# Performance work log

Measured on AMD Instinct MI355X. Metric: run time of the kernel, lower is better.

## Reference

```python
import jax, jax.numpy as jnp
import numpy as np

HIDDEN = 2048
N_HEADS = 16
N_KV_HEADS = 4
HEAD_DIM = HIDDEN // N_HEADS  # 128
ROPE_THETA = 10000.0
BATCH = 2
SEQ = 2048


def setup_inputs() -> dict:
    key = jax.random.key(0)
    k1, k2, k3, k4, k5 = jax.random.split(key, 5)
    s = 0.02
    return {
        "hidden_states": jax.random.normal(k1, (BATCH, SEQ, HIDDEN), dtype=jnp.float32),
        "attention_mask": jnp.zeros((BATCH, 1, 1, SEQ), dtype=jnp.float32),
        "Wq": jax.random.normal(k2, (HIDDEN, N_HEADS * HEAD_DIM), dtype=jnp.float32) * s,
        "Wk": jax.random.normal(k3, (HIDDEN, N_KV_HEADS * HEAD_DIM), dtype=jnp.float32) * s,
        "Wv": jax.random.normal(k4, (HIDDEN, N_KV_HEADS * HEAD_DIM), dtype=jnp.float32) * s,
        "Wo": jax.random.normal(k5, (N_HEADS * HEAD_DIM, HIDDEN), dtype=jnp.float32) * s,
    }


def _rope_cos_sin(seq_len, dtype):
    inv_freq = 1.0 / (ROPE_THETA ** (jnp.arange(0, HEAD_DIM, 2, dtype=jnp.float32) / HEAD_DIM))
    t = jnp.arange(seq_len, dtype=jnp.float32)
    freqs = t[:, None] * inv_freq[None, :]            # [S, D/2]
    emb = jnp.concatenate([freqs, freqs], axis=-1)    # [S, D]
    cos = jnp.cos(emb)[None, None, :, :].astype(dtype)  # [1,1,S,D]
    sin = jnp.sin(emb)[None, None, :, :].astype(dtype)
    return cos, sin


def _apply_rope(x, cos, sin):
    # x: [B,H,S,D]; faithful to torch code: rotated = cat((-x[...,1::2], x[...,::2]), -1)
    x1 = x[..., ::2]
    x2 = x[..., 1::2]
    rotated = jnp.concatenate([-x2, x1], axis=-1)
    return x * cos + rotated * sin


def reference(hidden_states, attention_mask, Wq, Wk, Wv, Wo):
    B, S, _ = hidden_states.shape
    scale = HEAD_DIM ** -0.5

    q = (hidden_states @ Wq).reshape(B, S, N_HEADS, HEAD_DIM).transpose(0, 2, 1, 3)      # [B,H,S,D]
    k = (hidden_states @ Wk).reshape(B, S, N_KV_HEADS, HEAD_DIM).transpose(0, 2, 1, 3)   # [B,KV,S,D]
    v = (hidden_states @ Wv).reshape(B, S, N_KV_HEADS, HEAD_DIM).transpose(0, 2, 1, 3)

    cos, sin = _rope_cos_sin(S, hidden_states.dtype)
    q = _apply_rope(q, cos, sin)
    k = _apply_rope(k, cos, sin)

    rep = N_HEADS // N_KV_HEADS
    k = jnp.repeat(k, rep, axis=1)  # [B,H,S,D]
    v = jnp.repeat(v, rep, axis=1)

    scores = jnp.einsum("bhqd,bhkd->bhqk", q, k) * scale  # [B,H,S,S]
    causal = jnp.tril(jnp.ones((S, S), dtype=bool))[None, None]
    scores = jnp.where(causal, scores, -jnp.inf)
    scores = scores + attention_mask  # additive float mask, broadcast [B,1,1,S]

    attn = jax.nn.softmax(scores, axis=-1)
    out = jnp.einsum("bhqk,bhkd->bhqd", attn, v)           # [B,H,S,D]
    out = out.transpose(0, 2, 1, 3).reshape(B, S, N_HEADS * HEAD_DIM)
    return out @ Wo
```

## Files before the change

### kernel.cpp

```cpp
#include <hip/hip_runtime.h>
#include <hip/hip_bf16.h>

#define BATCH 2
#define SEQ   2048
#define NH    16
#define NKV   4
#define HD    128
#define KDIM  2048
#define MROWS 4096
#define NQKV  3072

typedef __attribute__((ext_vector_type(8))) short  s16x8;
typedef __attribute__((ext_vector_type(4))) short  s16x4;
typedef __attribute__((ext_vector_type(4))) float  f32x4;
typedef __attribute__((ext_vector_type(8))) __bf16 b16x8;

#define BARRIER_LDS() do { \
    asm volatile("s_waitcnt lgkmcnt(0)" ::: "memory"); \
    __builtin_amdgcn_s_barrier(); \
  } while (0)

__device__ __forceinline__ unsigned short f2bf(float f) {
  __hip_bfloat16 h = __float2bfloat16(f);
  return *reinterpret_cast<unsigned short*>(&h);
}
__device__ __forceinline__ float bf2f(unsigned short h) {
  union { unsigned int u; float f; } x; x.u = ((unsigned int)h) << 16;
  return x.f;
}

__device__ __forceinline__ f32x4 MFMA16(s16x8 a, s16x8 b, f32x4 c) {
  return __builtin_amdgcn_mfma_f32_16x16x32_bf16(
      __builtin_bit_cast(b16x8, a), __builtin_bit_cast(b16x8, b), c, 0, 0, 0);
}

__device__ __forceinline__ void gload_lds16(const void* g, void* lds) {
  __builtin_amdgcn_global_load_lds(
      (const __attribute__((address_space(1))) void*)g,
      (__attribute__((address_space(3))) void*)lds, 16, 0, 0);
}

__global__ __launch_bounds__(256) void transpose_convert(
    const float* __restrict__ W, unsigned short* __restrict__ WT, int Kd, int Nd) {
  __shared__ float tile[32][33];
  int n0 = blockIdx.x * 32, k0 = blockIdx.y * 32;
  int tx = threadIdx.x & 31, ty = threadIdx.x >> 5;
#pragma unroll
  for (int i = 0; i < 4; ++i)
    tile[ty + i * 8][tx] = W[(size_t)(k0 + ty + i * 8) * Nd + n0 + tx];
  __syncthreads();
#pragma unroll
  for (int i = 0; i < 4; ++i)
    WT[(size_t)(n0 + ty + i * 8) * Kd + k0 + tx] = f2bf(tile[tx][ty + i * 8]);
}

__global__ __launch_bounds__(256) void conv_bf16(
    const float* __restrict__ X, unsigned short* __restrict__ Y) {
  int i = blockIdx.x * 256 + threadIdx.x;
  const float4 a = ((const float4*)X)[2 * i];
  const float4 b = ((const float4*)X)[2 * i + 1];
  s16x8 o;
  o[0] = (short)f2bf(a.x); o[1] = (short)f2bf(a.y);
  o[2] = (short)f2bf(a.z); o[3] = (short)f2bf(a.w);
  o[4] = (short)f2bf(b.x); o[5] = (short)f2bf(b.y);
  o[6] = (short)f2bf(b.z); o[7] = (short)f2bf(b.w);
  ((s16x8*)Y)[i] = o;
}

__global__ __launch_bounds__(256) void rope_table_kernel(float* __restrict__ tbl) {
  int i = blockIdx.x * 256 + threadIdx.x;
  int s = i >> 6, j = i & 63;
  float inv = powf(10000.0f, -(float)(2 * j) * (1.0f / 128.0f));
  float f = (float)s * inv;
  tbl[2 * i]     = cosf(f);
  tbl[2 * i + 1] = sinf(f);
}

__global__ __launch_bounds__(256) void gemm_qkv(
    const unsigned short* __restrict__ A, const unsigned short* __restrict__ BT,
    unsigned short* __restrict__ Qo, unsigned short* __restrict__ Ko,
    unsigned short* __restrict__ Vo) {
  __shared__ __align__(16) unsigned short la[128][32];
  __shared__ __align__(16) unsigned short lb[128][32];
  int tid = threadIdx.x, lane = tid & 63, w = tid >> 6;
  int lin = blockIdx.x;
  int swz = (lin & 7) * 96 + (lin >> 3);
  int bx = swz % 24, by = swz / 24;
  int m0 = by * 128, n0 = bx * 128;
  int wr = (w >> 1) * 64, wc = (w & 1) * 64;
  int fr = lane & 15, kg = (lane >> 4) * 8, rg = (lane >> 4) * 4;
  f32x4 acc[4][4] = {};
  for (int kt = 0; kt < KDIM; kt += 32) {
    __syncthreads();
#pragma unroll
    for (int i = 0; i < 2; ++i) {
      int idx = tid + i * 256;
      int row = idx >> 2, seg = idx & 3;
      gload_lds16(A + (size_t)(m0 + row) * KDIM + kt + seg * 8,
                  (char*)la + (size_t)(i * 256 + w * 64) * 16);
      gload_lds16(BT + (size_t)(n0 + row) * KDIM + kt + seg * 8,
                  (char*)lb + (size_t)(i * 256 + w * 64) * 16);
    }
    __syncthreads();
    s16x8 af[4], bf[4];
#pragma unroll
    for (int mi = 0; mi < 4; ++mi) af[mi] = *(const s16x8*)(&la[wr + mi * 16 + fr][kg]);
#pragma unroll
    for (int ni = 0; ni < 4; ++ni) bf[ni] = *(const s16x8*)(&lb[wc + ni * 16 + fr][kg]);
#pragma unroll
    for (int mi = 0; mi < 4; ++mi)
#pragma unroll
      for (int ni = 0; ni < 4; ++ni) acc[mi][ni] = MFMA16(af[mi], bf[ni], acc[mi][ni]);
  }
  int rbase = m0 + wr + rg;
#pragma unroll
  for (int ni = 0; ni < 4; ++ni) {
    int gn = n0 + wc + ni * 16 + fr;
    if (gn < 2048) {
      int hh = gn >> 7, d = gn & 127;
#pragma unroll
      for (int mi = 0; mi < 4; ++mi)
#pragma unroll
        for (int r = 0; r < 4; ++r) {
          int grow = rbase + mi * 16 + r;
          int bb = grow >> 11, ss = grow & 2047;
          Qo[((size_t)(bb * NH + hh) * SEQ + ss) * HD + d] = f2bf(acc[mi][ni][r]);
        }
    } else if (gn < 2560) {
      int c = gn - 2048, kvh = c >> 7, d = c & 127;
#pragma unroll
      for (int mi = 0; mi < 4; ++mi)
#pragma unroll
        for (int r = 0; r < 4; ++r) {
          int grow = rbase + mi * 16 + r;
          int bb = grow >> 11, ss = grow & 2047;
          Ko[((size_t)(bb * NKV + kvh) * SEQ + ss) * HD + d] = f2bf(acc[mi][ni][r]);
        }
    } else {
      int c = gn - 2560, kvh = c >> 7, d = c & 127;
#pragma unroll
      for (int mi = 0; mi < 4; ++mi) {
        int grow0 = rbase + mi * 16;
        int bb = grow0 >> 11, ss = grow0 & 2047;
        s16x4 pk;
#pragma unroll
        for (int r = 0; r < 4; ++r) pk[r] = (short)f2bf(acc[mi][ni][r]);
        *(s16x4*)(Vo + ((size_t)(bb * NKV + kvh) * HD + d) * SEQ + ss) = pk;
      }
    }
  }
}

__global__ __launch_bounds__(256) void gemm_out(
    const unsigned short* __restrict__ A, const unsigned short* __restrict__ BT,
    float* __restrict__ C) {
  __shared__ __align__(16) unsigned short la[128][32];
  __shared__ __align__(16) unsigned short lb[128][32];
  int tid = threadIdx.x, lane = tid & 63, w = tid >> 6;
  int lin = blockIdx.x;
  int swz = (lin & 7) * 64 + (lin >> 3);
  int bx = swz % 16, by = swz / 16;
  int m0 = by * 128, n0 = bx * 128;
  int wr = (w >> 1) * 64, wc = (w & 1) * 64;
  int fr = lane & 15, kg = (lane >> 4) * 8, rg = (lane >> 4) * 4;
  f32x4 acc[4][4] = {};
  for (int kt = 0; kt < KDIM; kt += 32) {
    __syncthreads();
#pragma unroll
    for (int i = 0; i < 2; ++i) {
      int idx = tid + i * 256;
      int row = idx >> 2, seg = idx & 3;
      gload_lds16(A + (size_t)(m0 + row) * KDIM + kt + seg * 8,
                  (char*)la + (size_t)(i * 256 + w * 64) * 16);
      gload_lds16(BT + (size_t)(n0 + row) * KDIM + kt + seg * 8,
                  (char*)lb + (size_t)(i * 256 + w * 64) * 16);
    }
    __syncthreads();
    s16x8 af[4], bf[4];
#pragma unroll
    for (int mi = 0; mi < 4; ++mi) af[mi] = *(const s16x8*)(&la[wr + mi * 16 + fr][kg]);
#pragma unroll
    for (int ni = 0; ni < 4; ++ni) bf[ni] = *(const s16x8*)(&lb[wc + ni * 16 + fr][kg]);
#pragma unroll
    for (int mi = 0; mi < 4; ++mi)
#pragma unroll
      for (int ni = 0; ni < 4; ++ni) acc[mi][ni] = MFMA16(af[mi], bf[ni], acc[mi][ni]);
  }
  int rbase = m0 + wr + rg;
#pragma unroll
  for (int ni = 0; ni < 4; ++ni) {
    int gn = n0 + wc + ni * 16 + fr;
#pragma unroll
    for (int mi = 0; mi < 4; ++mi)
#pragma unroll
      for (int r = 0; r < 4; ++r)
        C[(size_t)(rbase + mi * 16 + r) * 2048 + gn] = acc[mi][ni][r];
  }
}

__global__ __launch_bounds__(256) void rope2(
    unsigned short* __restrict__ X, const float* __restrict__ tbl) {
  __shared__ __align__(16) unsigned short xs[32][136];
  int tid = threadIdx.x;
  size_t r0 = (size_t)blockIdx.x * 32;
#pragma unroll
  for (int i = 0; i < 2; ++i) {
    int idx = tid + i * 256;
    int pr = idx >> 4, seg = idx & 15;
    *(s16x8*)(&xs[pr][seg * 8]) = *(const s16x8*)(X + (r0 + pr) * 128 + seg * 8);
  }
  __syncthreads();
  int pr = tid >> 3, jb = (tid & 7) * 8;
  size_t row = r0 + pr;
  int s = (int)(row & (SEQ - 1));
  s16x8 o0, o1;
#pragma unroll
  for (int j0 = 0; j0 < 8; ++j0) {
    int j = jb + j0;
    float c  = tbl[(s * 64 + j) * 2];
    float sn = tbl[(s * 64 + j) * 2 + 1];
    float xj   = bf2f(xs[pr][j]);
    float xj64 = bf2f(xs[pr][j + 64]);
    float x2j  = bf2f(xs[pr][2 * j]);
    float x2j1 = bf2f(xs[pr][2 * j + 1]);
    o0[j0] = (short)f2bf(xj * c - x2j1 * sn);
    o1[j0] = (short)f2bf(xj64 * c + x2j * sn);
  }
  unsigned short* xp = X + row * 128;
  *(s16x8*)(xp + jb)      = o0;
  *(s16x8*)(xp + 64 + jb) = o1;
}

__global__ __launch_bounds__(256, 2) void attn_fwd(
    const unsigned short* __restrict__ Q, const unsigned short* __restrict__ K,
    const unsigned short* __restrict__ VT, const float* __restrict__ mask,
    unsigned short* __restrict__ O) {
  __shared__ __align__(16) unsigned short kt_[64][136];
  __shared__ __align__(16) unsigned short vt_[128][68];
  __shared__ __align__(16) unsigned short pt_[4][16][36];

  int tid = threadIdx.x, lane = tid & 63, w = tid >> 6;
  int l = blockIdx.x;
  int grp = l & 7, slot = l >> 3;
  int hloc = slot & 3, qt = 31 - (slot >> 2);
  int b = grp >> 2, kvh = grp & 3, h = kvh * 4 + hloc;
  int qbase = qt * 64;
  int qw = qbase + w * 16;
  int fr = lane & 15, g = lane >> 4, kg = g * 8, rg = g * 4;

  const unsigned short* Qb = Q + (size_t)(b * NH + h) * SEQ * HD;
  const unsigned short* Kb = K + (size_t)(b * NKV + kvh) * SEQ * HD;
  const unsigned short* Vb = VT + (size_t)(b * NKV + kvh) * HD * SEQ;
  const float* mb = mask + (size_t)b * SEQ;

  int krow = tid >> 4, kpos = (tid & 15) * 8;
  const float sc2 = 0.12751744584812722f;
  const float L2E = 1.44269504088896f;
  int bS = b * SEQ;
  int ntiles = qt + 1;

  s16x8 aq[4];
#pragma unroll
  for (int dc = 0; dc < 4; ++dc)
    aq[dc] = *(const s16x8*)(Qb + (size_t)(qw + fr) * HD + dc * 32 + kg);

  f32x4 oacc[8] = {};
  float m_r = -3e38f, l_r = 0.f;

  s16x8 kreg[4], vreg[4];
#pragma unroll
  for (int i = 0; i < 4; ++i)
    kreg[i] = *(const s16x8*)(Kb + (size_t)(krow + i * 16) * HD + kpos);
#pragma unroll
  for (int i = 0; i < 4; ++i) {
    int c = tid + 256 * i;
    vreg[i] = *(const s16x8*)(Vb + (size_t)(c >> 3) * SEQ + (c & 7) * 8);
  }
#pragma unroll
  for (int i = 0; i < 4; ++i)
    *(s16x8*)(&kt_[krow + i * 16][kpos]) = kreg[i];
  BARRIER_LDS();

  for (int t = 0; t < ntiles; ++t) {
    int kv0 = t * 64;
    bool notlast = (t + 1 < ntiles);
    bool diag = (kv0 + 63 > qw);

#pragma unroll
    for (int i = 0; i < 4; ++i) {
      int c = tid + 256 * i;
      *(s16x8*)(&vt_[c >> 3][(c & 7) * 8]) = vreg[i];
    }
    if (notlast) {
#pragma unroll
      for (int i = 0; i < 4; ++i)
        kreg[i] = *(const s16x8*)(Kb + (size_t)(kv0 + 64 + krow + i * 16) * HD + kpos);
    }

    f32x4 sf[4];
    __builtin_amdgcn_s_setprio(1);
#pragma unroll
    for (int mk = 0; mk < 4; ++mk) {
      s16x8 ak[4];
#pragma unroll
      for (int dc = 0; dc < 4; ++dc)
        ak[dc] = *(const s16x8*)(&kt_[mk * 16 + fr][dc * 32 + kg]);
      sf[mk] = f32x4{0.f, 0.f, 0.f, 0.f};
#pragma unroll
      for (int dc = 0; dc < 4; ++dc)
        sf[mk] = MFMA16(ak[dc], aq[dc], sf[mk]);
    }
    __builtin_amdgcn_s_setprio(0);

#pragma unroll
    for (int mk = 0; mk < 4; ++mk) {
      float4 mv = *(const float4*)(mb + kv0 + mk * 16 + rg);
      float mvr[4] = {mv.x * L2E, mv.y * L2E, mv.z * L2E, mv.w * L2E};
      if (diag) {
#pragma unroll
        for (int r = 0; r < 4; ++r) {
          int kv = kv0 + mk * 16 + rg + r;
          float v = sf[mk][r] * sc2 + mvr[r];
          sf[mk][r] = (kv <= qw + fr) ? v : -3e38f;
        }
      } else {
#pragma unroll
        for (int r = 0; r < 4; ++r)
          sf[mk][r] = sf[mk][r] * sc2 + mvr[r];
      }
    }

    float pm01a = fmaxf(sf[0][0], sf[0][1]), pm01b = fmaxf(sf[0][2], sf[0][3]);
    float pm11a = fmaxf(sf[1][0], sf[1][1]), pm11b = fmaxf(sf[1][2], sf[1][3]);
    float pm21a = fmaxf(sf[2][0], sf[2][1]), pm21b = fmaxf(sf[2][2], sf[2][3]);
    float pm31a = fmaxf(sf[3][0], sf[3][1]), pm31b = fmaxf(sf[3][2], sf[3][3]);
    float pm0 = fmaxf(pm01a, pm01b), pm1 = fmaxf(pm11a, pm11b);
    float pm2 = fmaxf(pm21a, pm21b), pm3 = fmaxf(pm31a, pm31b);
    float pm = fmaxf(fmaxf(pm0, pm1), fmaxf(pm2, pm3));
    pm = fmaxf(pm, __shfl_xor(pm, 16, 64));
    pm = fmaxf(pm, __shfl_xor(pm, 32, 64));
    if (!__all(pm - m_r <= 8.0f)) {
      float mo = m_r;
      float mn = fmaxf(mo, pm);
      float al = exp2f(mo - mn);
      m_r = mn;
      l_r *= al;
#pragma unroll
      for (int r = 0; r < 4; ++r) {
        float ar = __shfl(al, rg + r, 16);
#pragma unroll
        for (int od = 0; od < 8; ++od) oacc[od][r] *= ar;
      }
    }
    float rs = 0.f;
#pragma unroll
    for (int mk = 0; mk < 4; ++mk)
#pragma unroll
      for (int r = 0; r < 4; ++r) {
        float ppv = exp2f(sf[mk][r] - m_r);
        sf[mk][r] = ppv;
        rs += ppv;
      }
    rs += __shfl_xor(rs, 16, 64);
    rs += __shfl_xor(rs, 32, 64);
    l_r += rs;

    BARRIER_LDS();

    if (notlast) {
#pragma unroll
      for (int i = 0; i < 4; ++i)
        *(s16x8*)(&kt_[krow + i * 16][kpos]) = kreg[i];
#pragma unroll
      for (int i = 0; i < 4; ++i) {
        int c = tid + 256 * i;
        vreg[i] = *(const s16x8*)(Vb + (size_t)(c >> 3) * SEQ + kv0 + 64 + (c & 7) * 8);
      }
    }

#pragma unroll
    for (int kk = 0; kk < 2; ++kk) {
#pragma unroll
      for (int mh = 0; mh < 2; ++mh) {
        int mk = kk * 2 + mh;
        s16x4 pk;
#pragma unroll
        for (int r = 0; r < 4; ++r) pk[r] = (short)f2bf(sf[mk][r]);
        *(s16x4*)(&pt_[w][fr][mh * 16 + rg]) = pk;
      }
      s16x8 ap = *(const s16x8*)(&pt_[w][fr][kg]);
      __builtin_amdgcn_s_setprio(1);
#pragma unroll
      for (int od = 0; od < 8; ++od) {
        s16x8 bv = *(const s16x8*)(&vt_[od * 16 + fr][kk * 32 + kg]);
        oacc[od] = MFMA16(ap, bv, oacc[od]);
      }
      __builtin_amdgcn_s_setprio(0);
    }
    BARRIER_LDS();
  }

  float iv = 1.0f / l_r;
  float ivr[4];
#pragma unroll
  for (int r = 0; r < 4; ++r) ivr[r] = __shfl(iv, rg + r, 16);
#pragma unroll
  for (int r = 0; r < 4; ++r) {
    unsigned short* op = O + (size_t)(bS + qw + rg + r) * 2048 + h * 128 + fr;
#pragma unroll
    for (int od = 0; od < 8; ++od)
      op[od * 16] = f2bf(oacc[od][r] * ivr[r]);
  }
}

extern "C" void kernel_launch(void* const* d_in, const int* in_sizes, int n_in,
                              void* d_out, int out_size, void* d_ws, size_t ws_size,
                              hipStream_t stream) {
  const float* hidden = (const float*)d_in[0];
  const float* mask   = (const float*)d_in[1];
  const float* Wq     = (const float*)d_in[2];
  const float* Wk     = (const float*)d_in[3];
  const float* Wv     = (const float*)d_in[4];
  const float* Wo     = (const float*)d_in[5];
  float* out = (float*)d_out;

  char* ws = (char*)d_ws;
  unsigned short* BT  = (unsigned short*)(ws);
  unsigned short* WoT = (unsigned short*)(ws + 12582912);
  unsigned short* Qb  = (unsigned short*)(ws + 20971520);
  unsigned short* Kb  = (unsigned short*)(ws + 37748736);
  unsigned short* VT  = (unsigned short*)(ws + 41943040);
  unsigned short* AO  = (unsigned short*)(ws + 46137344);
  float*          tbl = (float*)(ws + 62914560);
  unsigned short* Ab  = AO;

  conv_bf16<<<MROWS * KDIM / (256 * 8), 256, 0, stream>>>(hidden, Ab);
  transpose_convert<<<dim3(64, 64), 256, 0, stream>>>(Wq, BT, KDIM, 2048);
  transpose_convert<<<dim3(16, 64), 256, 0, stream>>>(Wk, BT + (size_t)2048 * KDIM, KDIM, 512);
  transpose_convert<<<dim3(16, 64), 256, 0, stream>>>(Wv, BT + (size_t)2560 * KDIM, KDIM, 512);
  transpose_convert<<<dim3(64, 64), 256, 0, stream>>>(Wo, WoT, KDIM, 2048);
  rope_table_kernel<<<512, 256, 0, stream>>>(tbl);

  gemm_qkv<<<dim3(768), 256, 0, stream>>>(Ab, BT, Qb, Kb, VT);
  rope2<<<(BATCH * NH * SEQ) / 32, 256, 0, stream>>>(Qb, tbl);
  rope2<<<(BATCH * NKV * SEQ) / 32, 256, 0, stream>>>(Kb, tbl);
  attn_fwd<<<dim3(1024), 256, 0, stream>>>(Qb, Kb, VT, mask, AO);
  gemm_out<<<dim3(512), 256, 0, stream>>>(AO, WoT, out);
}
```

Baseline: 229.3 us.

## Double-buffer K/V tiles in attention and merge weight-prep and rope launches

The attention kernel now keeps two LDS buffers for K and V. The next tile is written into the spare buffer while the current one is consumed, which removes one of the two block barriers per iteration. The four weight transpose launches are merged into a single grid, and the two rope launches into another, to cut launch overhead. Doubling the LDS footprint per block (to about 70KB) may limit occupancy under the requested two blocks per CU.

Measured after the change: 228.4 us. About the same (-0.4%).

```diff
diff --git a/kernel.cpp b/kernel.cpp
--- a/kernel.cpp
+++ b/kernel.cpp
@@ -40,10 +40,18 @@
       (__attribute__((address_space(3))) void*)lds, 16, 0, 0);
 }
 
-__global__ __launch_bounds__(256) void transpose_convert(
-    const float* __restrict__ W, unsigned short* __restrict__ WT, int Kd, int Nd) {
+__global__ __launch_bounds__(256) void prep_weights(
+    const float* __restrict__ Wq, const float* __restrict__ Wk,
+    const float* __restrict__ Wv, const float* __restrict__ Wo,
+    unsigned short* __restrict__ BT, unsigned short* __restrict__ WoT) {
   __shared__ float tile[32][33];
-  int n0 = blockIdx.x * 32, k0 = blockIdx.y * 32;
+  int bx = blockIdx.x;
+  const float* W; unsigned short* WT; int Nd, nb;
+  if (bx < 64)       { W = Wq; WT = BT;                          Nd = 2048; nb = bx; }
+  else if (bx < 80)  { W = Wk; WT = BT + (size_t)2048 * KDIM;    Nd = 512;  nb = bx - 64; }
+  else if (bx < 96)  { W = Wv; WT = BT + (size_t)2560 * KDIM;    Nd = 512;  nb = bx - 80; }
+  else               { W = Wo; WT = WoT;                         Nd = 2048; nb = bx - 96; }
+  int n0 = nb * 32, k0 = blockIdx.y * 32;
   int tx = threadIdx.x & 31, ty = threadIdx.x >> 5;
 #pragma unroll
   for (int i = 0; i < 4; ++i)
@@ -51,7 +59,7 @@
   __syncthreads();
 #pragma unroll
   for (int i = 0; i < 4; ++i)
-    WT[(size_t)(n0 + ty + i * 8) * Kd + k0 + tx] = f2bf(tile[tx][ty + i * 8]);
+    WT[(size_t)(n0 + ty + i * 8) * KDIM + k0 + tx] = f2bf(tile[tx][ty + i * 8]);
 }
 
 __global__ __launch_bounds__(256) void conv_bf16(
@@ -199,10 +207,15 @@
 }
 
 __global__ __launch_bounds__(256) void rope2(
-    unsigned short* __restrict__ X, const float* __restrict__ tbl) {
+    unsigned short* __restrict__ Qx, unsigned short* __restrict__ Kx,
+    const float* __restrict__ tbl) {
   __shared__ __align__(16) unsigned short xs[32][136];
   int tid = threadIdx.x;
-  size_t r0 = (size_t)blockIdx.x * 32;
+  int bid = blockIdx.x;
+  unsigned short* X;
+  size_t r0;
+  if (bid < 2048) { X = Qx; r0 = (size_t)bid * 32; }
+  else            { X = Kx; r0 = (size_t)(bid - 2048) * 32; }
 #pragma unroll
   for (int i = 0; i < 2; ++i) {
     int idx = tid + i * 256;
@@ -235,8 +248,8 @@
     const unsigned short* __restrict__ Q, const unsigned short* __restrict__ K,
     const unsigned short* __restrict__ VT, const float* __restrict__ mask,
     unsigned short* __restrict__ O) {
-  __shared__ __align__(16) unsigned short kt_[64][136];
-  __shared__ __align__(16) unsigned short vt_[128][68];
+  __shared__ __align__(16) unsigned short kt_[2][64][136];
+  __shared__ __align__(16) unsigned short vt_[2][128][68];
   __shared__ __align__(16) unsigned short pt_[4][16][36];
 
   int tid = threadIdx.x, lane = tid & 63, w = tid >> 6;
@@ -254,6 +267,7 @@
   const float* mb = mask + (size_t)b * SEQ;
 
   int krow = tid >> 4, kpos = (tid & 15) * 8;
+  int vrow0 = tid >> 3, vcol = (tid & 7) * 8;
   const float sc2 = 0.12751744584812722f;
   const float L2E = 1.44269504088896f;
   int bS = b * SEQ;
@@ -278,23 +292,48 @@
   }
 #pragma unroll
   for (int i = 0; i < 4; ++i)
-    *(s16x8*)(&kt_[krow + i * 16][kpos]) = kreg[i];
+    *(s16x8*)(&kt_[0][krow + i * 16][kpos]) = kreg[i];
+#pragma unroll
+  for (int i = 0; i < 4; ++i) {
+    int c = tid + 256 * i;
+    *(s16x8*)(&vt_[0][c >> 3][(c & 7) * 8]) = vreg[i];
+  }
+  if (ntiles > 1) {
+#pragma unroll
+    for (int i = 0; i < 4; ++i)
+      kreg[i] = *(const s16x8*)(Kb + (size_t)(64 + krow + i * 16) * HD + kpos);
+#pragma unroll
+    for (int i = 0; i < 4; ++i) {
+      int c = tid + 256 * i;
+      vreg[i] = *(const s16x8*)(Vb + (size_t)(c >> 3) * SEQ + 64 + (c & 7) * 8);
+    }
+  }
   BARRIER_LDS();
 
   for (int t = 0; t < ntiles; ++t) {
     int kv0 = t * 64;
-    bool notlast = (t + 1 < ntiles);
-    bool diag = (kv0 + 63 > qw);
-
-#pragma unroll
-    for (int i = 0; i < 4; ++i) {
-      int c = tid + 256 * i;
-      *(s16x8*)(&vt_[c >> 3][(c & 7) * 8]) = vreg[i];
-    }
-    if (notlast) {
+    int cur = t & 1;
+    bool diag = (t == qt);
+
+    if (t + 1 < ntiles) {
 #pragma unroll
       for (int i = 0; i < 4; ++i)
-        kreg[i] = *(const s16x8*)(Kb + (size_t)(kv0 + 64 + krow + i * 16) * HD + kpos);
+        *(s16x8*)(&kt_[cur ^ 1][krow + i * 16][kpos]) = kreg[i];
+#pragma unroll
+      for (int i = 0; i < 4; ++i) {
+        int c = tid + 256 * i;
+        *(s16x8*)(&vt_[cur ^ 1][c >> 3][(c & 7) * 8]) = vreg[i];
+      }
+      if (t + 2 < ntiles) {
+#pragma unroll
+        for (int i = 0; i < 4; ++i)
+          kreg[i] = *(const s16x8*)(Kb + (size_t)(kv0 + 128 + krow + i * 16) * HD + kpos);
+#pragma unroll
+        for (int i = 0; i < 4; ++i) {
+          int c = tid + 256 * i;
+          vreg[i] = *(const s16x8*)(Vb + (size_t)(c >> 3) * SEQ + kv0 + 128 + (c & 7) * 8);
+        }
+      }
     }
 
     f32x4 sf[4];
@@ -304,7 +343,7 @@
       s16x8 ak[4];
 #pragma unroll
       for (int dc = 0; dc < 4; ++dc)
-        ak[dc] = *(const s16x8*)(&kt_[mk * 16 + fr][dc * 32 + kg]);
+        ak[dc] = *(const s16x8*)(&kt_[cur][mk * 16 + fr][dc * 32 + kg]);
       sf[mk] = f32x4{0.f, 0.f, 0.f, 0.f};
 #pragma unroll
       for (int dc = 0; dc < 4; ++dc)
@@ -365,19 +404,6 @@
     rs += __shfl_xor(rs, 32, 64);
     l_r += rs;
 
-    BARRIER_LDS();
-
-    if (notlast) {
-#pragma unroll
-      for (int i = 0; i < 4; ++i)
-        *(s16x8*)(&kt_[krow + i * 16][kpos]) = kreg[i];
-#pragma unroll
-      for (int i = 0; i < 4; ++i) {
-        int c = tid + 256 * i;
-        vreg[i] = *(const s16x8*)(Vb + (size_t)(c >> 3) * SEQ + kv0 + 64 + (c & 7) * 8);
-      }
-    }
-
 #pragma unroll
     for (int kk = 0; kk < 2; ++kk) {
 #pragma unroll
@@ -392,11 +418,12 @@
       __builtin_amdgcn_s_setprio(1);
 #pragma unroll
       for (int od = 0; od < 8; ++od) {
-        s16x8 bv = *(const s16x8*)(&vt_[od * 16 + fr][kk * 32 + kg]);
+        s16x8 bv = *(const s16x8*)(&vt_[cur][od * 16 + fr][kk * 32 + kg]);
         oacc[od] = MFMA16(ap, bv, oacc[od]);
       }
       __builtin_amdgcn_s_setprio(0);
     }
+
     BARRIER_LDS();
   }
 
@@ -435,15 +462,11 @@
   unsigned short* Ab  = AO;
 
   conv_bf16<<<MROWS * KDIM / (256 * 8), 256, 0, stream>>>(hidden, Ab);
-  transpose_convert<<<dim3(64, 64), 256, 0, stream>>>(Wq, BT, KDIM, 2048);
-  transpose_convert<<<dim3(16, 64), 256, 0, stream>>>(Wk, BT + (size_t)2048 * KDIM, KDIM, 512);
-  transpose_convert<<<dim3(16, 64), 256, 0, stream>>>(Wv, BT + (size_t)2560 * KDIM, KDIM, 512);
-  transpose_convert<<<dim3(64, 64), 256, 0, stream>>>(Wo, WoT, KDIM, 2048);
+  prep_weights<<<dim3(160, 64), 256, 0, stream>>>(Wq, Wk, Wv, Wo, BT, WoT);
   rope_table_kernel<<<512, 256, 0, stream>>>(tbl);
 
   gemm_qkv<<<dim3(768), 256, 0, stream>>>(Ab, BT, Qb, Kb, VT);
-  rope2<<<(BATCH * NH * SEQ) / 32, 256, 0, stream>>>(Qb, tbl);
-  rope2<<<(BATCH * NKV * SEQ) / 32, 256, 0, stream>>>(Kb, tbl);
+  rope2<<<dim3(2048 + 512), 256, 0, stream>>>(Qb, Kb, tbl);
   attn_fwd<<<dim3(1024), 256, 0, stream>>>(Qb, Kb, VT, mask, AO);
   gemm_out<<<dim3(512), 256, 0, stream>>>(AO, WoT, out);
 }
```
